# Performance work log

Hardware: AMD Instinct MI355X
Metric: run time of the kernel (lower is better)

## Reference

```python
import jax, jax.numpy as jnp
import numpy as np

DIM = 1024
HEADS = 16
HEAD_DIM = DIM // HEADS
SCALE = HEAD_DIM ** -0.5
KSIZES = (1, 3, 5)


def setup_inputs() -> dict:
    key = jax.random.key(0)
    ks = jax.random.split(key, 16)
    b, n = 2, 2048
    s = 0.02
    inp = {
        "x": jax.random.normal(ks[0], (b, n, DIM), jnp.float32),
        "Wq": jax.random.normal(ks[1], (DIM, DIM), jnp.float32) * s,
        "Wk": jax.random.normal(ks[2], (DIM, DIM), jnp.float32) * s,
        "Wv": jax.random.normal(ks[3], (DIM, DIM), jnp.float32) * s,
        "Wo": jax.random.normal(ks[4], (DIM, DIM), jnp.float32) * s,
        "bo": jnp.zeros((DIM,), jnp.float32),
        "temperature": jnp.ones((1, HEADS, 1, 1), jnp.float32),
        "head_weights": jnp.ones((1, HEADS, 1, 1), jnp.float32),
    }
    # grouped Conv1d kernels: (out_ch=DIM, in_ch_per_group=DIM//HEADS, k)
    for i, k in enumerate(KSIZES):
        inp[f"conv_w{k}"] = jax.random.normal(ks[5 + i], (DIM, DIM // HEADS, k), jnp.float32) * s
        inp[f"conv_b{k}"] = jnp.zeros((DIM,), jnp.float32)
    return inp


def _grouped_conv1d(x_bdn, w, b, k):
    # x_bdn: [b, dim, n]; w: [dim, dim//HEADS, k]; 'same' padding for odd k
    y = jax.lax.conv_general_dilated(
        x_bdn, w, window_strides=(1,), padding=[(k // 2, k // 2)],
        dimension_numbers=("NCH", "OIH", "NCH"), feature_group_count=HEADS)
    return y + b[None, :, None]


def reference(x, Wq, Wk, Wv, Wo, bo, temperature, head_weights,
              conv_w1, conv_b1, conv_w3, conv_b3, conv_w5, conv_b5):
    b, n, _ = x.shape
    split = lambda t: t.reshape(b, n, HEADS, HEAD_DIM).transpose(0, 2, 1, 3)  # b h n d
    q = split(x @ Wq.T)
    k = split(x @ Wk.T)
    v = split(x @ Wv.T)
    dots = jnp.einsum("bhnd,bhmd->bhnm", q, k) * SCALE * temperature
    attn = jax.nn.softmax(dots, axis=-1)
    attn = attn * jax.nn.softmax(head_weights, axis=1)
    out = jnp.einsum("bhnm,bhmd->bhnd", attn, v)
    out = out.transpose(0, 2, 1, 3).reshape(b, n, DIM)  # b n (h d)
    oc = out.transpose(0, 2, 1)  # b dim n
    conv_sum = (_grouped_conv1d(oc, conv_w1, conv_b1, 1)
                + _grouped_conv1d(oc, conv_w3, conv_b3, 3)
                + _grouped_conv1d(oc, conv_w5, conv_b5, 5))
    n_scales = float(len(KSIZES))
    out_combined = out + conv_sum.transpose(0, 2, 1) / n_scales
    return out_combined @ Wo.T + bo
```

## Files before the change

### kernel.cpp

```cpp
#include <hip/hip_runtime.h>

#define DIM 1024
#define HEADS 16
#define HD 64
#define BATCH 2
#define SEQ 2048
#define MROWS (BATCH * SEQ)

typedef short s16x8 __attribute__((ext_vector_type(8)));
typedef short s16x4 __attribute__((ext_vector_type(4)));
typedef float f32x4 __attribute__((ext_vector_type(4)));
typedef float f32x16 __attribute__((ext_vector_type(16)));
typedef unsigned u32x4 __attribute__((ext_vector_type(4)));

__device__ __forceinline__ short f2bf(float f) {
  unsigned u = __builtin_bit_cast(unsigned, f);
  u = u + 0x7fffu + ((u >> 16) & 1u);
  return (short)(u >> 16);
}

__device__ __forceinline__ float bf2f(short s) {
  unsigned u = ((unsigned)(unsigned short)s) << 16;
  return __builtin_bit_cast(float, u);
}

__device__ __forceinline__ float fexp2(float x) { return __builtin_amdgcn_exp2f(x); }

__device__ __forceinline__ unsigned cvtpk(float lo, float hi) {
  unsigned r;
  asm("v_cvt_pk_bf16_f32 %0, %1, %2" : "=v"(r) : "v"(lo), "v"(hi));
  return r;
}

__device__ __forceinline__ void gload16(const void* g, void* l) {
  __builtin_amdgcn_global_load_lds((__attribute__((address_space(1))) void*)g,
                                   (__attribute__((address_space(3))) void*)l,
                                   16, 0, 0);
}

__global__ __launch_bounds__(256) void cvt_bf16(const float* __restrict__ in,
                                                short* __restrict__ out, int n4) {
  int i = blockIdx.x * 256 + threadIdx.x;
  if (i >= n4) return;
  f32x4 v = *(const f32x4*)(in + (size_t)i * 4);
  s16x4 o;
#pragma unroll
  for (int j = 0; j < 4; ++j) o[j] = f2bf(v[j]);
  *(s16x4*)(out + (size_t)i * 4) = o;
}

__global__ __launch_bounds__(256)
void cvt_w4(const float* __restrict__ a, const float* __restrict__ b,
            const float* __restrict__ c, const float* __restrict__ d,
            short* __restrict__ oa, short* __restrict__ ob, short* __restrict__ oc,
            short* __restrict__ od) {
  int k = blockIdx.y;
  const float* in = (k == 0) ? a : (k == 1) ? b : (k == 2) ? c : d;
  short* out = (k == 0) ? oa : (k == 1) ? ob : (k == 2) ? oc : od;
  int i = blockIdx.x * 256 + threadIdx.x;
  f32x4 v = *(const f32x4*)(in + (size_t)i * 4);
  s16x4 o;
#pragma unroll
  for (int j = 0; j < 4; ++j) o[j] = f2bf(v[j]);
  *(s16x4*)(out + (size_t)i * 4) = o;
}

#define QSTAGE(BUF, KT)                                                                \
  _Pragma("unroll") for (int i = 0; i < 2; ++i) {                                      \
    int cbase = i * 512 + wave * 64;                                                   \
    int c = cbase + lane;                                                              \
    int row = c >> 3;                                                                  \
    int cb = ((c ^ row) & 7) << 4;                                                     \
    gload16((const char*)A + ((size_t)(brow + row) * DIM + (KT)) * 2 + cb,             \
            (char*)&As[BUF][0][0] + cbase * 16);                                       \
    gload16((const char*)Bq + ((size_t)(bcol + row) * DIM + (KT)) * 2 + cb,            \
            (char*)&Bs[BUF][0][0][0] + cbase * 16);                                    \
    gload16((const char*)Bk + ((size_t)(bcol + row) * DIM + (KT)) * 2 + cb,            \
            (char*)&Bs[BUF][1][0][0] + cbase * 16);                                    \
    gload16((const char*)Bv + ((size_t)(bcol + row) * DIM + (KT)) * 2 + cb,            \
            (char*)&Bs[BUF][2][0][0] + cbase * 16);                                    \
  }

__global__ __launch_bounds__(512)
void qkv_fused(const short* __restrict__ A, const short* __restrict__ Bq,
               const short* __restrict__ Bk, const short* __restrict__ Bv,
               const float* __restrict__ scq, short* __restrict__ oq,
               short* __restrict__ ok, short* __restrict__ ov) {
  __shared__ __align__(16) short As[2][128][64];
  __shared__ __align__(16) short Bs[2][3][128][64];
  const int tid = threadIdx.x;
  const int lane = tid & 63, wave = tid >> 6;
  const int fr = lane & 15, fg = lane >> 4;
  const int wr = wave >> 1, wc = wave & 1;
  const int brow = blockIdx.y * 128, bcol = blockIdx.x * 128;

  int offA[2][2], offB[2][4];
#pragma unroll
  for (int kk = 0; kk < 2; ++kk) {
    int sw = ((kk * 4 + fg) ^ (fr & 7)) << 4;
#pragma unroll
    for (int m = 0; m < 2; ++m) offA[kk][m] = (wr * 32 + m * 16 + fr) * 128 + sw;
#pragma unroll
    for (int n = 0; n < 4; ++n) offB[kk][n] = (wc * 64 + n * 16 + fr) * 128 + sw;
  }

  f32x4 acc[3][2][4] = {};

  QSTAGE(0, 0);
  __syncthreads();

  for (int kt = 0; kt < DIM; kt += 64) {
    const int cur = (kt >> 6) & 1;
    if (kt + 64 < DIM) { QSTAGE(cur ^ 1, kt + 64); }
    const char* Ab = (const char*)&As[cur][0][0];
    const char* Bb = (const char*)&Bs[cur][0][0][0];
#pragma unroll
    for (int kk = 0; kk < 2; ++kk) {
      s16x8 af[2];
#pragma unroll
      for (int m = 0; m < 2; ++m) af[m] = *(const s16x8*)(Ab + offA[kk][m]);
#pragma unroll
      for (int z = 0; z < 3; ++z) {
        s16x8 bfr[4];
#pragma unroll
        for (int n = 0; n < 4; ++n) bfr[n] = *(const s16x8*)(Bb + z * 16384 + offB[kk][n]);
#pragma unroll
        for (int m = 0; m < 2; ++m)
#pragma unroll
          for (int n = 0; n < 4; ++n)
            acc[z][m][n] =
                __builtin_amdgcn_mfma_f32_16x16x32_bf16(af[m], bfr[n], acc[z][m][n], 0, 0, 0);
      }
    }
    __syncthreads();
  }

  const int hh = (bcol >> 6) + wc;
  const float sv = scq[hh];
#pragma unroll
  for (int m = 0; m < 2; ++m) {
#pragma unroll
    for (int n = 0; n < 4; ++n) {
      int i0 = brow + wr * 32 + m * 16 + fg * 4;
      int dd = n * 16 + fr;
#pragma unroll
      for (int r = 0; r < 4; ++r) {
        int i = i0 + r;
        size_t qko = (((size_t)(i >> 11) * HEADS + hh) * SEQ + (i & (SEQ - 1))) * HD + dd;
        oq[qko] = f2bf(acc[0][m][n][r] * sv);
        ok[qko] = f2bf(acc[1][m][n][r]);
      }
      s16x4 o4;
#pragma unroll
      for (int r = 0; r < 4; ++r) o4[r] = f2bf(acc[2][m][n][r]);
      *(s16x4*)&ov[(((size_t)(i0 >> 11) * HEADS + hh) * HD + dd) * SEQ + (i0 & (SEQ - 1))] = o4;
    }
  }
}

#define GSTAGE(BUF, KT)                                                              \
  _Pragma("unroll") for (int i = 0; i < 4; ++i) {                                    \
    int cbase = (wave * 4 + i) * 64;                                                 \
    int chunk = cbase + lane;                                                        \
    int row = chunk >> 3;                                                            \
    int cb = ((chunk ^ row) & 7) << 4;                                               \
    gload16((const char*)A + ((size_t)(brow + row) * DIM + (KT)) * 2 + cb,           \
            (char*)&As[BUF][0][0] + cbase * 16);                                     \
    gload16((const char*)Bw + ((size_t)(bcol + row) * DIM + (KT)) * 2 + cb,          \
            (char*)&Bs[BUF][0][0] + cbase * 16);                                     \
  }

__global__ __launch_bounds__(256)
void out_gemm(const short* __restrict__ A, const short* __restrict__ Bw,
              const float* __restrict__ bias, float* __restrict__ out) {
  __shared__ __align__(16) short As[2][128][64];
  __shared__ __align__(16) short Bs[2][128][64];
  const int tid = threadIdx.x;
  const int lane = tid & 63, wave = tid >> 6;
  const int fr = lane & 15, fg = lane >> 4;
  const int wr = wave >> 1, wc = wave & 1;
  const int brow = blockIdx.y * 128, bcol = blockIdx.x * 128;
  f32x4 acc[4][4] = {};

  int offA[2][4], offB[2][4];
#pragma unroll
  for (int kk = 0; kk < 2; ++kk)
#pragma unroll
    for (int f = 0; f < 4; ++f) {
      int sw = ((kk * 4 + fg) ^ (fr & 7)) << 4;
      offA[kk][f] = (wr * 64 + f * 16 + fr) * 128 + sw;
      offB[kk][f] = (wc * 64 + f * 16 + fr) * 128 + sw;
    }

  GSTAGE(0, 0);
  __syncthreads();

  for (int kt = 0; kt < DIM; kt += 64) {
    const int cur = (kt >> 6) & 1;
    if (kt + 64 < DIM) { GSTAGE(cur ^ 1, kt + 64); }
    const char* Ab = (const char*)&As[cur][0][0];
    const char* Bb = (const char*)&Bs[cur][0][0];
#pragma unroll
    for (int kk = 0; kk < 2; ++kk) {
      s16x8 af[4], bfr[4];
#pragma unroll
      for (int m = 0; m < 4; ++m) af[m] = *(const s16x8*)(Ab + offA[kk][m]);
#pragma unroll
      for (int n = 0; n < 4; ++n) bfr[n] = *(const s16x8*)(Bb + offB[kk][n]);
#pragma unroll
      for (int m = 0; m < 4; ++m)
#pragma unroll
        for (int n = 0; n < 4; ++n)
          acc[m][n] = __builtin_amdgcn_mfma_f32_16x16x32_bf16(af[m], bfr[n], acc[m][n], 0, 0, 0);
    }
    __syncthreads();
  }

#pragma unroll
  for (int m = 0; m < 4; ++m) {
#pragma unroll
    for (int n = 0; n < 4; ++n) {
      int i0 = brow + wr * 64 + m * 16 + fg * 4;
      int j = bcol + wc * 64 + n * 16 + fr;
#pragma unroll
      for (int r = 0; r < 4; ++r)
        out[(size_t)(i0 + r) * DIM + j] = acc[m][n][r] + bias[j];
    }
  }
}

#define STAGE(BUF, KT)                                                                   \
  gload16((const char*)K + (bhoff + (size_t)((KT) + srow0) * HD) * 2 + scs0,             \
          (char*)&Ks[BUF][0][0] + wb0);                                                  \
  gload16((const char*)K + (bhoff + (size_t)((KT) + srow1) * HD) * 2 + scs1,             \
          (char*)&Ks[BUF][0][0] + wb1);                                                  \
  gload16((const char*)Vt + (vbase + (size_t)srow0 * SEQ + (KT)) * 2 + scs0,             \
          (char*)&Vs[BUF][0][0] + wb0);                                                  \
  gload16((const char*)Vt + (vbase + (size_t)srow1 * SEQ + (KT)) * 2 + scs1,             \
          (char*)&Vs[BUF][0][0] + wb1);

#define SOFTPV(CUR, ST, KCB)                                                             \
  {                                                                                      \
    float p[16];                                                                         \
    _Pragma("unroll") for (int r = 0; r < 16; ++r) p[r] = fexp2(ST[r]);                  \
    lrow += ((p[0] + p[1]) + (p[2] + p[3])) + ((p[4] + p[5]) + (p[6] + p[7])) +          \
            ((p[8] + p[9]) + (p[10] + p[11])) + ((p[12] + p[13]) + (p[14] + p[15]));     \
    unsigned pk[8];                                                                      \
    _Pragma("unroll") for (int q4 = 0; q4 < 4; ++q4) {                                   \
      pk[q4 * 2] = cvtpk(p[q4 * 4 + 0], p[q4 * 4 + 1]);                                  \
      pk[q4 * 2 + 1] = cvtpk(p[q4 * 4 + 2], p[q4 * 4 + 3]);                              \
    }                                                                                    \
    _Pragma("unroll") for (int kcl = 0; kcl < 2; ++kcl) {                                \
      unsigned a0 = pk[kcl * 4 + 0], b0 = pk[kcl * 4 + 2];                               \
      unsigned a1 = pk[kcl * 4 + 1], b1 = pk[kcl * 4 + 3];                               \
      asm("v_permlane32_swap_b32 %0, %1" : "+v"(a0), "+v"(b0));                          \
      asm("v_permlane32_swap_b32 %0, %1" : "+v"(a1), "+v"(b1));                          \
      u32x4 pw;                                                                          \
      pw.x = a0; pw.y = a1; pw.z = b0; pw.w = b1;                                        \
      s16x8 pf = __builtin_bit_cast(s16x8, pw);                                          \
      const char* vb = (const char*)&Vs[CUR][0][0] + off[(KCB) + kcl];                   \
      s16x8 v0 = *(const s16x8*)vb;                                                      \
      s16x8 v1 = *(const s16x8*)(vb + 4096);                                             \
      __builtin_amdgcn_s_setprio(1);                                                     \
      oacc0 = __builtin_amdgcn_mfma_f32_32x32x16_bf16(pf, v0, oacc0, 0, 0, 0);           \
      oacc1 = __builtin_amdgcn_mfma_f32_32x32x16_bf16(pf, v1, oacc1, 0, 0, 0);           \
      __builtin_amdgcn_s_setprio(0);                                                     \
    }                                                                                    \
  }

#define ATTN_TILE(CUR, STG, KTSTG, DOSTAGE, WAITSTR)                                     \
  {                                                                                      \
    asm volatile("s_waitcnt " WAITSTR ::: "memory");                                     \
    __builtin_amdgcn_s_barrier();                                                        \
    asm volatile("" ::: "memory");                                                       \
    if (DOSTAGE) { STAGE(STG, KTSTG); }                                                  \
    f32x16 st0 = {}, st1 = {};                                                           \
    __builtin_amdgcn_s_setprio(1);                                                       \
    _Pragma("unroll") for (int dc = 0; dc < 4; ++dc) {                                   \
      const char* kb = (const char*)&Ks[CUR][0][0] + off[dc];                            \
      s16x8 k0 = *(const s16x8*)kb;                                                      \
      s16x8 k1 = *(const s16x8*)(kb + 4096);                                             \
      st0 = __builtin_amdgcn_mfma_f32_32x32x16_bf16(k0, qf[dc], st0, 0, 0, 0);           \
      st1 = __builtin_amdgcn_mfma_f32_32x32x16_bf16(k1, qf[dc], st1, 0, 0, 0);           \
    }                                                                                    \
    __builtin_amdgcn_s_setprio(0);                                                       \
    SOFTPV(CUR, st0, 0);                                                                 \
    SOFTPV(CUR, st1, 2);                                                                 \
  }

__global__ __launch_bounds__(256)
void attn_fwd(const short* __restrict__ Q, const short* __restrict__ K,
              const short* __restrict__ Vt, short* __restrict__ att,
              const float* __restrict__ hw) {
  __shared__ __align__(16) short Ks[3][64][64];
  __shared__ __align__(16) short Vs[3][64][64];
  const int bh = blockIdx.y;
  const int h = bh & (HEADS - 1);
  const int qbase = blockIdx.x * 128;
  const int tid = threadIdx.x;
  const int lane = tid & 63, wave = tid >> 6;
  const int l31 = lane & 31, hi = lane >> 5;

  float hmax = -1e30f;
  for (int i = 0; i < HEADS; ++i) hmax = fmaxf(hmax, hw[i]);
  float hsum = 0.f;
  for (int i = 0; i < HEADS; ++i) hsum += expf(hw[i] - hmax);
  const float hwsm = expf(hw[h] - hmax) / hsum;

  const size_t bhoff = (size_t)bh * SEQ * HD;
  const size_t vbase = (size_t)bh * HD * SEQ;
  const int qrow = qbase + wave * 32 + l31;

  s16x8 qf[4];
#pragma unroll
  for (int dc = 0; dc < 4; ++dc)
    qf[dc] = *(const s16x8*)&Q[bhoff + (size_t)qrow * HD + dc * 16 + hi * 8];

  int off[4];
#pragma unroll
  for (int c = 0; c < 4; ++c) off[c] = l31 * 128 + (((2 * c + hi) ^ (l31 & 7)) << 4);

  const int c0 = wave * 64 + lane;
  const int srow0 = c0 >> 3;
  const int scs0 = ((c0 & 7) ^ (srow0 & 7)) << 4;
  const int srow1 = srow0 + 32;
  const int scs1 = ((c0 & 7) ^ (srow1 & 7)) << 4;
  const int wb0 = wave * 1024, wb1 = 4096 + wave * 1024;

  f32x16 oacc0 = {}, oacc1 = {};
  float lrow = 0.f;

  STAGE(0, 0);
  STAGE(1, 64);

  for (int ktg = 0; ktg + 192 <= SEQ; ktg += 192) {
    ATTN_TILE(0, 2, ktg + 128, true, "vmcnt(4)");
    ATTN_TILE(1, 0, ktg + 192, true, "vmcnt(4)");
    ATTN_TILE(2, 1, ktg + 256, true, "vmcnt(4)");
  }
  ATTN_TILE(0, 0, 0, false, "vmcnt(4)");
  ATTN_TILE(1, 0, 0, false, "vmcnt(0)");

  lrow += __shfl_xor(lrow, 32);

  const int b = bh >> 4;
  const float isc = hwsm / lrow;
#pragma unroll
  for (int reg = 0; reg < 16; ++reg) {
    int q = (reg & 3) + 8 * (reg >> 2) + 4 * hi;
    float sc = __shfl(isc, q);
    size_t ro = ((size_t)b * SEQ + qbase + wave * 32 + q) * DIM + h * HD;
    att[ro + l31] = f2bf(oacc0[reg] * sc);
    att[ro + 32 + l31] = f2bf(oacc1[reg] * sc);
  }
}

__global__ __launch_bounds__(256)
void prep_weff(const float* __restrict__ w1, const float* __restrict__ b1,
               const float* __restrict__ w3, const float* __restrict__ b3,
               const float* __restrict__ w5, const float* __restrict__ b5,
               const float* __restrict__ temp, short* __restrict__ weff,
               float* __restrict__ bsum, float* __restrict__ scq) {
  int idx = blockIdx.x * 256 + threadIdx.x;
  if (idx >= DIM * 64) return;
  float t0 = w5[(size_t)idx * 5 + 0];
  float t1 = w5[(size_t)idx * 5 + 1] + w3[(size_t)idx * 3 + 0];
  float t2 = w5[(size_t)idx * 5 + 2] + w3[(size_t)idx * 3 + 1] + w1[idx];
  float t3 = w5[(size_t)idx * 5 + 3] + w3[(size_t)idx * 3 + 2];
  float t4 = w5[(size_t)idx * 5 + 4];
  weff[0 * DIM * 64 + idx] = f2bf(t0);
  weff[1 * DIM * 64 + idx] = f2bf(t1);
  weff[2 * DIM * 64 + idx] = f2bf(t2);
  weff[3 * DIM * 64 + idx] = f2bf(t3);
  weff[4 * DIM * 64 + idx] = f2bf(t4);
  if ((idx & 63) == 0) {
    int o = idx >> 6;
    bsum[o] = b1[o] + b3[o] + b5[o];
  }
  if (idx < HEADS) scq[idx] = 0.125f * temp[idx] * 1.44269504f;
}

#define CP 68
__global__ __launch_bounds__(256)
void conv_mfma(const short* __restrict__ attb, const short* __restrict__ weff,
               const float* __restrict__ bsum, short* __restrict__ comb) {
  __shared__ __align__(16) short As[132][CP];
  __shared__ __align__(16) short Ws[5][64][CP];
  const int b = blockIdx.z, g = blockIdx.y, n0 = blockIdx.x * 128;
  const int tid = threadIdx.x, lane = tid & 63, wave = tid >> 6;
  const int fr = lane & 15, fg = lane >> 4;

  const short* abase = attb + (size_t)b * SEQ * DIM + g * 64;
  for (int idx = tid; idx < 132 * 8; idx += 256) {
    int r = idx >> 3, cb = (idx & 7) * 8;
    int rn = n0 + r - 2;
    s16x8 v = {};
    if (rn >= 0 && rn < SEQ) v = *(const s16x8*)&abase[(size_t)rn * DIM + cb];
    *(s16x8*)&As[r][cb] = v;
  }
  for (int idx = tid; idx < 5 * 64 * 8; idx += 256) {
    int t = idx >> 9;
    int rem = idx & 511;
    int o = rem >> 3, cb = (rem & 7) * 8;
    s16x8 v = *(const s16x8*)&weff[((size_t)t * DIM + g * 64 + o) * 64 + cb];
    *(s16x8*)&Ws[t][o][cb] = v;
  }
  __syncthreads();

  f32x4 acc[2][4] = {};
#pragma unroll
  for (int dt = 0; dt < 5; ++dt) {
#pragma unroll
    for (int kk = 0; kk < 2; ++kk) {
      const int ko = kk * 32 + fg * 8;
      s16x8 af[2], bfr[4];
#pragma unroll
      for (int m = 0; m < 2; ++m)
        af[m] = *(const s16x8*)&As[wave * 32 + m * 16 + fr + dt][ko];
#pragma unroll
      for (int n = 0; n < 4; ++n) bfr[n] = *(const s16x8*)&Ws[dt][n * 16 + fr][ko];
#pragma unroll
      for (int m = 0; m < 2; ++m)
#pragma unroll
        for (int n = 0; n < 4; ++n)
          acc[m][n] = __builtin_amdgcn_mfma_f32_16x16x32_bf16(af[m], bfr[n], acc[m][n], 0, 0, 0);
    }
  }

#pragma unroll
  for (int m = 0; m < 2; ++m) {
#pragma unroll
    for (int n = 0; n < 4; ++n) {
      int lrow0 = wave * 32 + m * 16 + fg * 4;
      int col = n * 16 + fr;
      float bs = bsum[g * 64 + col];
#pragma unroll
      for (int r = 0; r < 4; ++r) {
        int lr = lrow0 + r;
        float res = bf2f(As[lr + 2][col]);
        float outv = res + (acc[m][n][r] + bs) * (1.f / 3.f);
        comb[((size_t)b * SEQ + n0 + lr) * DIM + g * 64 + col] = f2bf(outv);
      }
    }
  }
}

extern "C" void kernel_launch(void* const* d_in, const int* in_sizes, int n_in, void* d_out,
                              int out_size, void* d_ws, size_t ws_size, hipStream_t stream) {
  const float* x = (const float*)d_in[0];
  const float* Wq = (const float*)d_in[1];
  const float* Wk = (const float*)d_in[2];
  const float* Wv = (const float*)d_in[3];
  const float* Wo = (const float*)d_in[4];
  const float* bo = (const float*)d_in[5];
  const float* temp = (const float*)d_in[6];
  const float* hw = (const float*)d_in[7];
  const float* w1 = (const float*)d_in[8];
  const float* b1 = (const float*)d_in[9];
  const float* w3 = (const float*)d_in[10];
  const float* b3 = (const float*)d_in[11];
  const float* w5 = (const float*)d_in[12];
  const float* b5 = (const float*)d_in[13];

  char* ws = (char*)d_ws;
  const size_t MB = 1u << 20;
  short* xb = (short*)(ws);
  short* wqb = (short*)(ws + 8 * MB);
  short* wkb = (short*)(ws + 10 * MB);
  short* wvb = (short*)(ws + 12 * MB);
  short* wob = (short*)(ws + 14 * MB);
  short* qb = (short*)(ws + 16 * MB);
  short* kb = (short*)(ws + 24 * MB);
  short* vtb = (short*)(ws + 32 * MB);
  short* attb = (short*)(ws + 40 * MB);
  short* comb = (short*)(ws + 48 * MB);
  short* weff = (short*)(ws + 56 * MB);
  float* bsum = (float*)(ws + 57 * MB);
  float* scq = (float*)(ws + 57 * MB + 4096);

  cvt_bf16<<<4096, 256, 0, stream>>>(x, xb, (MROWS * DIM) / 4);
  cvt_w4<<<dim3(1024, 4), 256, 0, stream>>>(Wq, Wk, Wv, Wo, wqb, wkb, wvb, wob);
  prep_weff<<<256, 256, 0, stream>>>(w1, b1, w3, b3, w5, b5, temp, weff, bsum, scq);

  qkv_fused<<<dim3(DIM / 128, MROWS / 128), 512, 0, stream>>>(xb, wqb, wkb, wvb, scq, qb, kb, vtb);

  attn_fwd<<<dim3(SEQ / 128, BATCH * HEADS), 256, 0, stream>>>(qb, kb, vtb, attb, hw);

  conv_mfma<<<dim3(SEQ / 128, HEADS, BATCH), 256, 0, stream>>>(attb, weff, bsum, comb);

  dim3 go(DIM / 128, MROWS / 128);
  out_gemm<<<go, 256, 0, stream>>>(comb, wob, bo, (float*)d_out);
}
```

Before: 124.1 us.

## Software-pipeline attention: overlap next tile QK^T with current softmax/PV

Restructures the attention inner loop so each step computes QK^T scores for tile t while doing softmax and PV for tile t-1, using double-buffered score registers and a 4-deep LDS ring instead of 3. The goal is to let MFMA work on the next tile's scores hide the exp/convert/permlane latency of the softmax. The cost is more registers for the extra score accumulators and more LDS, which may reduce occupancy. The loop bounds are hand-unrolled for SEQ=2048.

After: 123.0 us. No clear change (-0.9%).

```diff
diff --git a/kernel.cpp b/kernel.cpp
--- a/kernel.cpp
+++ b/kernel.cpp
@@ -239,7 +239,26 @@
   gload16((const char*)Vt + (vbase + (size_t)srow1 * SEQ + (KT)) * 2 + scs1,             \
           (char*)&Vs[BUF][0][0] + wb1);
 
-#define SOFTPV(CUR, ST, KCB)                                                             \
+#define QKT(BUF, S0, S1)                                                                 \
+  {                                                                                      \
+    const char* kb0 = (const char*)&Ks[BUF][0][0];                                       \
+    __builtin_amdgcn_s_setprio(1);                                                       \
+    {                                                                                    \
+      s16x8 ka = *(const s16x8*)(kb0 + off[0]);                                          \
+      s16x8 kc = *(const s16x8*)(kb0 + off[0] + 4096);                                   \
+      S0 = __builtin_amdgcn_mfma_f32_32x32x16_bf16(ka, qf[0], zv, 0, 0, 0);              \
+      S1 = __builtin_amdgcn_mfma_f32_32x32x16_bf16(kc, qf[0], zv, 0, 0, 0);              \
+    }                                                                                    \
+    _Pragma("unroll") for (int dc = 1; dc < 4; ++dc) {                                   \
+      s16x8 ka = *(const s16x8*)(kb0 + off[dc]);                                         \
+      s16x8 kc = *(const s16x8*)(kb0 + off[dc] + 4096);                                  \
+      S0 = __builtin_amdgcn_mfma_f32_32x32x16_bf16(ka, qf[dc], S0, 0, 0, 0);             \
+      S1 = __builtin_amdgcn_mfma_f32_32x32x16_bf16(kc, qf[dc], S1, 0, 0, 0);             \
+    }                                                                                    \
+    __builtin_amdgcn_s_setprio(0);                                                       \
+  }
+
+#define SOFTPV(VBUF, ST, KCB)                                                            \
   {                                                                                      \
     float p[16];                                                                         \
     _Pragma("unroll") for (int r = 0; r < 16; ++r) p[r] = fexp2(ST[r]);                  \
@@ -258,7 +277,7 @@
       u32x4 pw;                                                                          \
       pw.x = a0; pw.y = a1; pw.z = b0; pw.w = b1;                                        \
       s16x8 pf = __builtin_bit_cast(s16x8, pw);                                          \
-      const char* vb = (const char*)&Vs[CUR][0][0] + off[(KCB) + kcl];                   \
+      const char* vb = (const char*)&Vs[VBUF][0][0] + off[(KCB) + kcl];                  \
       s16x8 v0 = *(const s16x8*)vb;                                                      \
       s16x8 v1 = *(const s16x8*)(vb + 4096);                                             \
       __builtin_amdgcn_s_setprio(1);                                                     \
@@ -268,32 +287,22 @@
     }                                                                                    \
   }
 
-#define ATTN_TILE(CUR, STG, KTSTG, DOSTAGE, WAITSTR)                                     \
+#define ASTEP(QKB, PVB, SC0, SC1, SP0, SP1, DOSTG, STGB, KTSTG, WAITSTR, DOPV)           \
   {                                                                                      \
     asm volatile("s_waitcnt " WAITSTR ::: "memory");                                     \
     __builtin_amdgcn_s_barrier();                                                        \
     asm volatile("" ::: "memory");                                                       \
-    if (DOSTAGE) { STAGE(STG, KTSTG); }                                                  \
-    f32x16 st0 = {}, st1 = {};                                                           \
-    __builtin_amdgcn_s_setprio(1);                                                       \
-    _Pragma("unroll") for (int dc = 0; dc < 4; ++dc) {                                   \
-      const char* kb = (const char*)&Ks[CUR][0][0] + off[dc];                            \
-      s16x8 k0 = *(const s16x8*)kb;                                                      \
-      s16x8 k1 = *(const s16x8*)(kb + 4096);                                             \
-      st0 = __builtin_amdgcn_mfma_f32_32x32x16_bf16(k0, qf[dc], st0, 0, 0, 0);           \
-      st1 = __builtin_amdgcn_mfma_f32_32x32x16_bf16(k1, qf[dc], st1, 0, 0, 0);           \
-    }                                                                                    \
-    __builtin_amdgcn_s_setprio(0);                                                       \
-    SOFTPV(CUR, st0, 0);                                                                 \
-    SOFTPV(CUR, st1, 2);                                                                 \
+    if (DOSTG) { STAGE(STGB, KTSTG); }                                                   \
+    QKT(QKB, SC0, SC1);                                                                  \
+    if (DOPV) { SOFTPV(PVB, SP0, 0); SOFTPV(PVB, SP1, 2); }                              \
   }
 
 __global__ __launch_bounds__(256)
 void attn_fwd(const short* __restrict__ Q, const short* __restrict__ K,
               const short* __restrict__ Vt, short* __restrict__ att,
               const float* __restrict__ hw) {
-  __shared__ __align__(16) short Ks[3][64][64];
-  __shared__ __align__(16) short Vs[3][64][64];
+  __shared__ __align__(16) short Ks[4][64][64];
+  __shared__ __align__(16) short Vs[4][64][64];
   const int bh = blockIdx.y;
   const int h = bh & (HEADS - 1);
   const int qbase = blockIdx.x * 128;
@@ -327,19 +336,31 @@
   const int scs1 = ((c0 & 7) ^ (srow1 & 7)) << 4;
   const int wb0 = wave * 1024, wb1 = 4096 + wave * 1024;
 
+  const f32x16 zv = {};
   f32x16 oacc0 = {}, oacc1 = {};
+  f32x16 sA0, sA1, sB0, sB1;
   float lrow = 0.f;
 
   STAGE(0, 0);
   STAGE(1, 64);
 
-  for (int ktg = 0; ktg + 192 <= SEQ; ktg += 192) {
-    ATTN_TILE(0, 2, ktg + 128, true, "vmcnt(4)");
-    ATTN_TILE(1, 0, ktg + 192, true, "vmcnt(4)");
-    ATTN_TILE(2, 1, ktg + 256, true, "vmcnt(4)");
-  }
-  ATTN_TILE(0, 0, 0, false, "vmcnt(4)");
-  ATTN_TILE(1, 0, 0, false, "vmcnt(0)");
+  ASTEP(0, 3, sA0, sA1, sB0, sB1, true, 2, 128, "vmcnt(4)", false);
+  ASTEP(1, 0, sB0, sB1, sA0, sA1, true, 3, 192, "vmcnt(4)", true);
+  ASTEP(2, 1, sA0, sA1, sB0, sB1, true, 0, 256, "vmcnt(4)", true);
+  ASTEP(3, 2, sB0, sB1, sA0, sA1, true, 1, 320, "vmcnt(4)", true);
+  for (int g = 1; g <= 6; ++g) {
+    const int kt = g * 256;
+    ASTEP(0, 3, sA0, sA1, sB0, sB1, true, 2, kt + 128, "vmcnt(4)", true);
+    ASTEP(1, 0, sB0, sB1, sA0, sA1, true, 3, kt + 192, "vmcnt(4)", true);
+    ASTEP(2, 1, sA0, sA1, sB0, sB1, true, 0, kt + 256, "vmcnt(4)", true);
+    ASTEP(3, 2, sB0, sB1, sA0, sA1, true, 1, kt + 320, "vmcnt(4)", true);
+  }
+  ASTEP(0, 3, sA0, sA1, sB0, sB1, true, 2, 1920, "vmcnt(4)", true);
+  ASTEP(1, 0, sB0, sB1, sA0, sA1, true, 3, 1984, "vmcnt(4)", true);
+  ASTEP(2, 1, sA0, sA1, sB0, sB1, false, 0, 0, "vmcnt(4)", true);
+  ASTEP(3, 2, sB0, sB1, sA0, sA1, false, 0, 0, "vmcnt(0)", true);
+  SOFTPV(3, sB0, 0);
+  SOFTPV(3, sB1, 2);
 
   lrow += __shfl_xor(lrow, 32);
 
```
